# Performance work log

Hardware: AMD Instinct MI355X
Metric: run time of the kernel (lower is better)

## Reference

```python
import jax, jax.numpy as jnp
import numpy as np

D_MODEL, D_HIDDEN, N_EXPERTS = 1024, 4096, 8
CAP_FACTOR, LBL_COEF, ZLOSS_COEF = 1.25, 0.01, 0.0


def setup_inputs() -> dict:
    key = jax.random.key(0)
    ks = jax.random.split(key, 4)
    B, T = 4, 2048
    x = jax.random.normal(ks[0], (B, T, D_MODEL), dtype=jnp.float32)
    # router linear
    Wr = jax.random.normal(ks[1], (D_MODEL, N_EXPERTS), jnp.float32) / np.sqrt(D_MODEL).astype(np.float32)
    br = jnp.zeros((N_EXPERTS,), jnp.float32)
    # per-expert MLP: fc1 [D->H], gelu, fc2 [H->D]
    W1 = jax.random.normal(ks[2], (N_EXPERTS, D_MODEL, D_HIDDEN), jnp.float32) / np.sqrt(D_MODEL).astype(np.float32)
    b1 = jnp.zeros((N_EXPERTS, D_HIDDEN), jnp.float32)
    W2 = jax.random.normal(ks[3], (N_EXPERTS, D_HIDDEN, D_MODEL), jnp.float32) / np.sqrt(D_HIDDEN).astype(np.float32)
    b2 = jnp.zeros((N_EXPERTS, D_MODEL), jnp.float32)
    return {"x": x, "Wr": Wr, "br": br, "W1": W1, "b1": b1, "W2": W2, "b2": b2}


def reference(x, Wr, br, W1, b1, W2, b2):
    B, T, D = x.shape
    N = B * T
    E = Wr.shape[1]
    cap = int(CAP_FACTOR * (N / E) + 1)  # static Python int

    h = x.reshape(N, D)
    # --- Top1Router ---
    logits = h @ Wr + br                              # [N, E]
    probs = jax.nn.softmax(logits, axis=-1)
    top1 = jnp.argmax(probs, axis=-1)                 # [N]
    w = jnp.take_along_axis(probs, top1[:, None], axis=1)  # [N, 1]
    assign = jax.nn.one_hot(top1, E, dtype=jnp.float32)    # constant wrt grads
    importance = probs.mean(axis=0)
    load = jax.lax.stop_gradient(assign).mean(axis=0)
    lb_loss = E * jnp.sum(importance * load)
    z_loss = jnp.mean(jax.nn.logsumexp(logits, axis=-1) ** 2)

    # --- capacity-based dispatch (first `cap` tokens per expert, token order) ---
    pos = (jnp.cumsum(assign, axis=0) * assign).sum(axis=-1).astype(jnp.int32) - 1  # [N] slot within expert
    keep = pos < cap
    slot = jnp.where(keep, pos, cap)  # dropped tokens -> overflow slot `cap`
    xe = jnp.zeros((E, cap + 1, D), x.dtype).at[top1, slot].set(h)[:, :cap]  # [E, cap, D]

    # --- per-expert MLP as grouped GEMMs ---
    he = jax.nn.gelu(jnp.einsum('ecd,edh->ech', xe, W1) + b1[:, None, :])    # [E, cap, H]
    ye = jnp.einsum('ech,ehd->ecd', he, W2) + b2[:, None, :]                 # [E, cap, D]

    # --- combine (gather back, scale by router weight, zero dropped) ---
    out = ye[top1, jnp.minimum(pos, cap - 1)] * w   # [N, D]
    out = jnp.where(keep[:, None], out, jnp.zeros((), x.dtype))
    y = out.reshape(B, T, D)
    aux = LBL_COEF * lb_loss + ZLOSS_COEF * z_loss
    return (y, aux)
```

## Files before the change

kernel.cpp:

```cpp
#include <hip/hip_runtime.h>
#include <hip/hip_bf16.h>

#define N_TOK 8192
#define DM    1024
#define DH    4096
#define NE    8
#define CAP   1281
#define CAPR  1408

typedef unsigned short u16;
typedef __attribute__((ext_vector_type(8))) __bf16 bf16x8;
typedef __attribute__((ext_vector_type(8))) short short8;
typedef __attribute__((ext_vector_type(4))) float f4;

__device__ __forceinline__ u16 f2bf(float f){
  union { float f; unsigned u; } v; v.f = f;
  unsigned r = v.u + 0x7fffu + ((v.u >> 16) & 1u);
  return (u16)(r >> 16);
}

__device__ __forceinline__ float gelu_t(float v){
  return 0.5f * v * (1.f + tanhf(0.7978845608028654f * (v + 0.044715f * v * v * v)));
}

__device__ __forceinline__ void gl2lds16(const void* g, void* l){
  __builtin_amdgcn_global_load_lds((const __attribute__((address_space(1))) void*)g,
                                   (__attribute__((address_space(3))) void*)l, 16, 0, 0);
}

__global__ __launch_bounds__(256) void cvt_x_k(const float* __restrict__ in, u16* __restrict__ out){
  int i = blockIdx.x * 256 + threadIdx.x;
  const f4* p = (const f4*)in + (size_t)i * 2;
  f4 a = p[0], b = p[1];
  short8 o;
  o[0]=(short)f2bf(a[0]); o[1]=(short)f2bf(a[1]); o[2]=(short)f2bf(a[2]); o[3]=(short)f2bf(a[3]);
  o[4]=(short)f2bf(b[0]); o[5]=(short)f2bf(b[1]); o[6]=(short)f2bf(b[2]); o[7]=(short)f2bf(b[3]);
  *(short8*)(out + (size_t)i*8) = o;
}

__global__ __launch_bounds__(256) void tcvt_k(const float* __restrict__ in, u16* __restrict__ out,
                                              int K, int Nn){
  __shared__ float tile[64][65];
  size_t mb = (size_t)blockIdx.z * (size_t)K * (size_t)Nn;
  const float* ip = in + mb;
  u16* op = out + mb;
  int n0 = blockIdx.x*64, k0 = blockIdx.y*64;
  int tx = threadIdx.x & 63, ty = threadIdx.x >> 6;
  #pragma unroll
  for (int i=0;i<16;i++){
    int r = ty*16 + i;
    tile[r][tx] = ip[(size_t)(k0+r)*Nn + n0 + tx];
  }
  __syncthreads();
  #pragma unroll
  for (int i=0;i<16;i++){
    int r = ty*16 + i;
    op[(size_t)(n0+r)*K + k0 + tx] = f2bf(tile[tx][r]);
  }
}

__global__ __launch_bounds__(256) void router_k(const float* __restrict__ x, const float* __restrict__ Wr,
    const float* __restrict__ br, int* __restrict__ top1, float* __restrict__ wgt,
    float* __restrict__ impSum){
  __shared__ float pSh[4][8];
  int wid = threadIdx.x >> 6, lane = threadIdx.x & 63;
  int n = blockIdx.x * 4 + wid;
  const float* xr = x + (size_t)n * DM;
  float acc[8];
  #pragma unroll
  for (int e=0;e<8;e++) acc[e]=0.f;
  #pragma unroll
  for (int c=0;c<4;c++){
    int d0 = c*256 + lane*4;
    f4 xv = *(const f4*)(xr + d0);
    #pragma unroll
    for (int j=0;j<4;j++){
      const float* wrow = Wr + (size_t)(d0+j)*NE;
      float xs = xv[j];
      #pragma unroll
      for (int e=0;e<8;e++) acc[e] = fmaf(xs, wrow[e], acc[e]);
    }
  }
  #pragma unroll
  for (int off=32; off>0; off>>=1){
    #pragma unroll
    for (int e=0;e<8;e++) acc[e] += __shfl_down(acc[e], off, 64);
  }
  if (lane==0){
    float lg[8]; float mx = -1e30f;
    #pragma unroll
    for (int e=0;e<8;e++){ lg[e] = acc[e] + br[e]; mx = fmaxf(mx, lg[e]); }
    float p[8], s=0.f;
    #pragma unroll
    for (int e=0;e<8;e++){ p[e] = expf(lg[e]-mx); s += p[e]; }
    int bt=0; float bv=lg[0];
    #pragma unroll
    for (int e=1;e<8;e++){ if (lg[e]>bv){ bv=lg[e]; bt=e; } }
    float inv = 1.f/s;
    top1[n] = bt; wgt[n] = p[bt]*inv;
    #pragma unroll
    for (int e=0;e<8;e++) pSh[wid][e] = p[e]*inv;
  }
  __syncthreads();
  if (threadIdx.x < 8){
    int e = threadIdx.x;
    atomicAdd(&impSum[e], pSh[0][e]+pSh[1][e]+pSh[2][e]+pSh[3][e]);
  }
}

__global__ __launch_bounds__(1024) void scan_k(const int* __restrict__ top1, int* __restrict__ idx,
    int* __restrict__ cnt, int* __restrict__ rawcnt, int* __restrict__ dropList,
    int* __restrict__ nDrop, const float* __restrict__ impSum, float* __restrict__ auxOut){
  __shared__ int waveCnt[16][8];
  __shared__ int wavePre[16][8];
  __shared__ int chunkTot[8];
  __shared__ int base_s[8];
  int tid = threadIdx.x, wid = tid>>6, lane = tid&63;
  if (tid < 8) base_s[tid] = 0;
  __syncthreads();
  for (int c=0;c<8;c++){
    int t = c*1024 + tid;
    int e = top1[t];
    int myPre = 0;
    #pragma unroll
    for (int ex=0; ex<8; ex++){
      unsigned long long mk = __ballot(e == ex);
      if (lane == 0) waveCnt[wid][ex] = __popcll(mk);
      if (ex == e) myPre = __popcll(mk & ((1ull<<lane)-1ull));
    }
    __syncthreads();
    if (tid < 8){
      int run = 0;
      for (int wv=0; wv<16; wv++){ wavePre[wv][tid] = run; run += waveCnt[wv][tid]; }
      chunkTot[tid] = run;
    }
    __syncthreads();
    int pos = base_s[e] + wavePre[wid][e] + myPre;
    if (pos < CAP) idx[e*CAPR + pos] = t;
    else { int d = atomicAdd(nDrop, 1); dropList[d] = t; }
    __syncthreads();
    if (tid < 8) base_s[tid] += chunkTot[tid];
    __syncthreads();
  }
  if (tid < 8){
    rawcnt[tid] = base_s[tid];
    cnt[tid] = base_s[tid] < CAP ? base_s[tid] : CAP;
  }
  if (tid == 0){
    float s = 0.f;
    for (int e=0;e<8;e++) s += (impSum[e]*(1.f/N_TOK)) * ((float)base_s[e]*(1.f/N_TOK));
    *auxOut = 0.01f * 8.f * s;
  }
}

__global__ __launch_bounds__(256) void zdrop_k(const int* __restrict__ dropList,
    const int* __restrict__ nDrop, float* __restrict__ y){
  int nd = *nDrop;
  for (int i = blockIdx.x; i < nd; i += gridDim.x){
    int t = dropList[i];
    f4* row = (f4*)(y + (size_t)t * DM);
    f4 z; z[0]=0.f; z[1]=0.f; z[2]=0.f; z[3]=0.f;
    row[threadIdx.x] = z;
  }
}

__global__ __launch_bounds__(256) void gemm1_k(
    const u16* __restrict__ Xb, const u16* __restrict__ W1T,
    const float* __restrict__ b1, const int* __restrict__ idx,
    const int* __restrict__ cnt, u16* __restrict__ He)
{
  int e = blockIdx.z, mt = blockIdx.y, nt = blockIdx.x;
  int cn = cnt[e];
  if (mt*128 >= cn) return;
  __shared__ __align__(16) u16 As[128*64];
  __shared__ __align__(16) u16 Bs[128*64];
  int tid = threadIdx.x, lane = tid&63, wid = tid>>6;
  int arow = tid>>3, acb = tid&7;

  const u16* aS[4]; const u16* bS[4];
  #pragma unroll
  for (int c=0;c<4;c++){
    int row = c*32 + arow;
    int gcb = acb ^ (row&7);
    int slot = mt*128 + row;
    int token = (slot < cn) ? idx[e*CAPR + slot] : idx[e*CAPR];
    aS[c] = Xb + (size_t)token*DM + gcb*8;
    bS[c] = W1T + ((size_t)e*DH + nt*128 + row)*DM + gcb*8;
  }
  f4 acc[4][4];
  #pragma unroll
  for (int m=0;m<4;m++)
    #pragma unroll
    for (int n=0;n<4;n++)
      #pragma unroll
      for (int j=0;j<4;j++) acc[m][n][j]=0.f;

  int waveM = wid>>1, waveN = wid&1;
  int rA = lane&15, kb = lane>>4;

  for (int kt=0; kt<DM/64; kt++){
    #pragma unroll
    for (int c=0;c<4;c++){
      gl2lds16(aS[c] + kt*64, &As[c*2048 + tid*8]);
      gl2lds16(bS[c] + kt*64, &Bs[c*2048 + tid*8]);
    }
    __syncthreads();
    #pragma unroll
    for (int kk=0;kk<2;kk++){
      bf16x8 af[4], bf_[4];
      #pragma unroll
      for (int m=0;m<4;m++){
        int row = waveM*64 + m*16 + rA;
        int ch = (kk*4+kb) ^ (row&7);
        af[m] = *(const bf16x8*)&As[row*64 + ch*8];
      }
      #pragma unroll
      for (int n=0;n<4;n++){
        int col = waveN*64 + n*16 + rA;
        int ch = (kk*4+kb) ^ (col&7);
        bf_[n] = *(const bf16x8*)&Bs[col*64 + ch*8];
      }
      #pragma unroll
      for (int m=0;m<4;m++)
        #pragma unroll
        for (int n=0;n<4;n++)
          acc[m][n] = __builtin_amdgcn_mfma_f32_16x16x32_bf16(af[m], bf_[n], acc[m][n], 0,0,0);
    }
    __syncthreads();
  }
  int rG = lane>>4;
  #pragma unroll
  for (int n=0;n<4;n++){
    int col = nt*128 + waveN*64 + n*16 + rA;
    float bias = b1[e*DH + col];
    #pragma unroll
    for (int m=0;m<4;m++){
      int slot = mt*128 + waveM*64 + m*16 + rG*4;
      u16* dst = He + ((size_t)e*CAPR + slot)*DH + col;
      #pragma unroll
      for (int j=0;j<4;j++){
        float v = acc[m][n][j] + bias;
        dst[(size_t)j*DH] = f2bf(gelu_t(v));
      }
    }
  }
}

__global__ __launch_bounds__(256) void gemm2_k(
    const u16* __restrict__ He, const u16* __restrict__ W2T,
    const float* __restrict__ b2, const int* __restrict__ idx,
    const int* __restrict__ cnt, const float* __restrict__ wgt,
    float* __restrict__ y)
{
  int e = blockIdx.z, mt = blockIdx.y, nt = blockIdx.x;
  int cn = cnt[e];
  if (mt*128 >= cn) return;
  __shared__ __align__(16) u16 As[128*64];
  __shared__ __align__(16) u16 Bs[128*64];
  int tid = threadIdx.x, lane = tid&63, wid = tid>>6;
  int arow = tid>>3, acb = tid&7;

  const u16* aS[4]; const u16* bS[4];
  #pragma unroll
  for (int c=0;c<4;c++){
    int row = c*32 + arow;
    int gcb = acb ^ (row&7);
    aS[c] = He  + ((size_t)e*CAPR + mt*128 + row)*DH + gcb*8;
    bS[c] = W2T + ((size_t)e*DM   + nt*128 + row)*DH + gcb*8;
  }
  f4 acc[4][4];
  #pragma unroll
  for (int m=0;m<4;m++)
    #pragma unroll
    for (int n=0;n<4;n++)
      #pragma unroll
      for (int j=0;j<4;j++) acc[m][n][j]=0.f;

  int waveM = wid>>1, waveN = wid&1;
  int rA = lane&15, kb = lane>>4;

  for (int kt=0; kt<DH/64; kt++){
    #pragma unroll
    for (int c=0;c<4;c++){
      gl2lds16(aS[c] + kt*64, &As[c*2048 + tid*8]);
      gl2lds16(bS[c] + kt*64, &Bs[c*2048 + tid*8]);
    }
    __syncthreads();
    #pragma unroll
    for (int kk=0;kk<2;kk++){
      bf16x8 af[4], bf_[4];
      #pragma unroll
      for (int m=0;m<4;m++){
        int row = waveM*64 + m*16 + rA;
        int ch = (kk*4+kb) ^ (row&7);
        af[m] = *(const bf16x8*)&As[row*64 + ch*8];
      }
      #pragma unroll
      for (int n=0;n<4;n++){
        int col = waveN*64 + n*16 + rA;
        int ch = (kk*4+kb) ^ (col&7);
        bf_[n] = *(const bf16x8*)&Bs[col*64 + ch*8];
      }
      #pragma unroll
      for (int m=0;m<4;m++)
        #pragma unroll
        for (int n=0;n<4;n++)
          acc[m][n] = __builtin_amdgcn_mfma_f32_16x16x32_bf16(af[m], bf_[n], acc[m][n], 0,0,0);
    }
    __syncthreads();
  }
  int rG = lane>>4;
  #pragma unroll
  for (int m=0;m<4;m++){
    int slot0 = mt*128 + waveM*64 + m*16 + rG*4;
    #pragma unroll
    for (int j=0;j<4;j++){
      int slot = slot0 + j;
      bool valid = slot < cn;
      int tk = valid ? idx[e*CAPR + slot] : 0;
      float wv = valid ? wgt[tk] : 0.f;
      #pragma unroll
      for (int n=0;n<4;n++){
        int col = nt*128 + waveN*64 + n*16 + rA;
        if (valid) y[(size_t)tk*DM + col] = (acc[m][n][j] + b2[e*DM + col]) * wv;
      }
    }
  }
}

extern "C" void kernel_launch(void* const* d_in, const int* in_sizes, int n_in,
                              void* d_out, int out_size, void* d_ws, size_t ws_size,
                              hipStream_t stream){
  const float* x  = (const float*)d_in[0];
  const float* Wr = (const float*)d_in[1];
  const float* br = (const float*)d_in[2];
  const float* W1 = (const float*)d_in[3];
  const float* b1 = (const float*)d_in[4];
  const float* W2 = (const float*)d_in[5];
  const float* b2 = (const float*)d_in[6];
  float* y = (float*)d_out;

  char* ws = (char*)d_ws;
  u16* Xb  = (u16*)(ws);
  u16* W1T = (u16*)(ws + 16777216ull);
  u16* W2T = (u16*)(ws + 16777216ull + 67108864ull);
  u16* He  = (u16*)(ws + 16777216ull + 2ull*67108864ull);
  char* tail = ws + 16777216ull + 2ull*67108864ull + (size_t)NE*CAPR*DH*2ull;
  int*   top1 = (int*)(tail);
  float* wgt  = (float*)(tail + 32768);
  int*   idx  = (int*)(tail + 65536);
  int*   drop = (int*)(tail + 65536 + 45056);
  float* impSum = (float*)(tail + 65536 + 45056 + 32768);
  int*   nDrop  = (int*)((char*)impSum + 32);
  int*   cnt    = nDrop + 1;
  int*   rawcnt = cnt + 8;

  hipMemsetAsync(impSum, 0, 64, stream);

  cvt_x_k<<<4096, 256, 0, stream>>>(x, Xb);
  tcvt_k<<<dim3(64,16,8), 256, 0, stream>>>(W1, W1T, DM, DH);
  tcvt_k<<<dim3(16,64,8), 256, 0, stream>>>(W2, W2T, DH, DM);
  router_k<<<2048, 256, 0, stream>>>(x, Wr, br, top1, wgt, impSum);
  scan_k<<<1, 1024, 0, stream>>>(top1, idx, cnt, rawcnt, drop, nDrop, impSum,
                                 y + (size_t)N_TOK*DM);
  zdrop_k<<<64, 256, 0, stream>>>(drop, nDrop, y);
  gemm1_k<<<dim3(DH/128, CAPR/128, NE), 256, 0, stream>>>(Xb, W1T, b1, idx, cnt, He);
  gemm2_k<<<dim3(DM/128, CAPR/128, NE), 256, 0, stream>>>(He, W2T, b2, idx, cnt, wgt, y);

  (void)in_sizes; (void)n_in; (void)out_size; (void)ws_size;
}
```

Baseline: 378.1 us.

## Double-buffer 256x256 grouped GEMMs with phased MFMA/load overlap and faster GELU

Both expert GEMMs move from 128x128 tiles with a single LDS buffer to 256x256 tiles on 512 threads. They double-buffer LDS and interleave global-to-LDS loads with MFMA phases, using explicit barriers, waitcnt and priority hints, so load latency hides behind compute. GELU's tanh is rewritten through exp and a hardware reciprocal, and the weight-transpose kernel now does vectorized loads and stores. The index array stride is padded to 1536 so the 6 larger M tiles can read past CAPR safely. The cost is higher register and LDS pressure, plus a slightly different GELU approximation.

```diff
diff --git a/kernel.cpp b/kernel.cpp
--- a/kernel.cpp
+++ b/kernel.cpp
@@ -7,6 +7,7 @@
 #define NE    8
 #define CAP   1281
 #define CAPR  1408
+#define ISTR  1536
 
 typedef unsigned short u16;
 typedef __attribute__((ext_vector_type(8))) __bf16 bf16x8;
@@ -19,8 +20,9 @@
   return (u16)(r >> 16);
 }
 
-__device__ __forceinline__ float gelu_t(float v){
-  return 0.5f * v * (1.f + tanhf(0.7978845608028654f * (v + 0.044715f * v * v * v)));
+__device__ __forceinline__ float gelu_fast(float v){
+  float u = 0.7978845608028654f * (v + 0.044715f * v * v * v);
+  return v * __builtin_amdgcn_rcpf(1.0f + __expf(-2.0f * u));
 }
 
 __device__ __forceinline__ void gl2lds16(const void* g, void* l){
@@ -40,23 +42,29 @@
 
 __global__ __launch_bounds__(256) void tcvt_k(const float* __restrict__ in, u16* __restrict__ out,
                                               int K, int Nn){
-  __shared__ float tile[64][65];
+  __shared__ float tile[64][68];
   size_t mb = (size_t)blockIdx.z * (size_t)K * (size_t)Nn;
   const float* ip = in + mb;
   u16* op = out + mb;
   int n0 = blockIdx.x*64, k0 = blockIdx.y*64;
-  int tx = threadIdx.x & 63, ty = threadIdx.x >> 6;
-  #pragma unroll
-  for (int i=0;i<16;i++){
-    int r = ty*16 + i;
-    tile[r][tx] = ip[(size_t)(k0+r)*Nn + n0 + tx];
+  int t = threadIdx.x;
+  int kr = t>>4, nc = (t&15)*4;
+  #pragma unroll
+  for (int ii=0;ii<4;ii++){
+    f4 v = *(const f4*)&ip[(size_t)(k0+kr+16*ii)*Nn + n0 + nc];
+    tile[kr+16*ii][nc+0] = v[0]; tile[kr+16*ii][nc+1] = v[1];
+    tile[kr+16*ii][nc+2] = v[2]; tile[kr+16*ii][nc+3] = v[3];
   }
   __syncthreads();
-  #pragma unroll
-  for (int i=0;i<16;i++){
-    int r = ty*16 + i;
-    op[(size_t)(n0+r)*K + k0 + tx] = f2bf(tile[tx][r]);
-  }
+  int nr = t>>2, kc = (t&3)*16;
+  short8 o0, o1;
+  #pragma unroll
+  for (int c=0;c<8;c++){
+    o0[c] = (short)f2bf(tile[kc+c][nr]);
+    o1[c] = (short)f2bf(tile[kc+8+c][nr]);
+  }
+  *(short8*)&op[(size_t)(n0+nr)*K + k0 + kc] = o0;
+  *(short8*)&op[(size_t)(n0+nr)*K + k0 + kc + 8] = o1;
 }
 
 __global__ __launch_bounds__(256) void router_k(const float* __restrict__ x, const float* __restrict__ Wr,
@@ -136,7 +144,7 @@
     }
     __syncthreads();
     int pos = base_s[e] + wavePre[wid][e] + myPre;
-    if (pos < CAP) idx[e*CAPR + pos] = t;
+    if (pos < CAP) idx[e*ISTR + pos] = t;
     else { int d = atomicAdd(nDrop, 1); dropList[d] = t; }
     __syncthreads();
     if (tid < 8) base_s[tid] += chunkTot[tid];
@@ -164,89 +172,119 @@
   }
 }
 
-__global__ __launch_bounds__(256) void gemm1_k(
+#define SA(buf, h, kt) do{ \
+  gl2lds16(aS[(h)*2+0] + (size_t)(kt)*64, &lds[(buf)*16384 + ((h)*2+0)*4096 + t*8]); \
+  gl2lds16(aS[(h)*2+1] + (size_t)(kt)*64, &lds[(buf)*16384 + ((h)*2+1)*4096 + t*8]); }while(0)
+#define SBg(buf, h, kt) do{ \
+  gl2lds16(bS[(h)*2+0] + (size_t)(kt)*64, &lds[32768 + (buf)*16384 + ((h)*2+0)*4096 + t*8]); \
+  gl2lds16(bS[(h)*2+1] + (size_t)(kt)*64, &lds[32768 + (buf)*16384 + ((h)*2+1)*4096 + t*8]); }while(0)
+
+#define LDA(buf, m, kk) (*(const bf16x8*)&lds[(buf)*16384 + (aBase ^ ((kk)*32)) + (m)*1024])
+#define LDB(buf, n, kk) (*(const bf16x8*)&lds[32768 + (buf)*16384 + (bBase ^ ((kk)*32)) + (n)*1024])
+
+#define PHASE(buf, q, STAGES, PREBAR) do{ \
+  bf16x8 a_[2][2]; \
+  if ((q)==0){ \
+    _Pragma("unroll") for (int n_=0;n_<4;n_++) \
+      _Pragma("unroll") for (int kk_=0;kk_<2;kk_++) Bf[n_][kk_] = LDB(buf, n_, kk_); \
+  } \
+  _Pragma("unroll") for (int j_=0;j_<2;j_++) \
+    _Pragma("unroll") for (int kk_=0;kk_<2;kk_++) a_[j_][kk_] = LDA(buf, 2*(q)+j_, kk_); \
+  STAGES; \
+  __builtin_amdgcn_s_barrier(); \
+  asm volatile("s_waitcnt lgkmcnt(0)" ::: "memory"); \
+  __builtin_amdgcn_sched_barrier(0); \
+  __builtin_amdgcn_s_setprio(1); \
+  _Pragma("unroll") for (int j_=0;j_<2;j_++) \
+    _Pragma("unroll") for (int n_=0;n_<4;n_++) \
+      _Pragma("unroll") for (int kk_=0;kk_<2;kk_++) \
+        acc[2*(q)+j_][n_] = __builtin_amdgcn_mfma_f32_16x16x32_bf16(a_[j_][kk_], Bf[n_][kk_], acc[2*(q)+j_][n_], 0,0,0); \
+  __builtin_amdgcn_s_setprio(0); \
+  PREBAR; \
+  __builtin_amdgcn_s_barrier(); \
+}while(0)
+
+#define VMC4 asm volatile("s_waitcnt vmcnt(4)" ::: "memory")
+#define NOP2 (void)0
+
+__global__ __launch_bounds__(512, 2) void gemm1_k(
     const u16* __restrict__ Xb, const u16* __restrict__ W1T,
     const float* __restrict__ b1, const int* __restrict__ idx,
     const int* __restrict__ cnt, u16* __restrict__ He)
 {
   int e = blockIdx.z, mt = blockIdx.y, nt = blockIdx.x;
   int cn = cnt[e];
-  if (mt*128 >= cn) return;
-  __shared__ __align__(16) u16 As[128*64];
-  __shared__ __align__(16) u16 Bs[128*64];
-  int tid = threadIdx.x, lane = tid&63, wid = tid>>6;
-  int arow = tid>>3, acb = tid&7;
+  if (mt*256 >= cn) return;
+  __shared__ __align__(16) u16 lds[65536];
+  int t = threadIdx.x, lane = t&63, wid = t>>6;
+  int waveM = wid>>2, waveN = wid&3;
+  int rA = lane&15, kb = lane>>4, s = rA&7;
 
   const u16* aS[4]; const u16* bS[4];
   #pragma unroll
-  for (int c=0;c<4;c++){
-    int row = c*32 + arow;
-    int gcb = acb ^ (row&7);
-    int slot = mt*128 + row;
-    int token = (slot < cn) ? idx[e*CAPR + slot] : idx[e*CAPR];
-    aS[c] = Xb + (size_t)token*DM + gcb*8;
-    bS[c] = W1T + ((size_t)e*DH + nt*128 + row)*DM + gcb*8;
-  }
-  f4 acc[4][4];
-  #pragma unroll
-  for (int m=0;m<4;m++)
+  for (int j=0;j<4;j++){
+    int pos = j*512 + t;
+    int row = pos>>3, ch = pos&7;
+    int gcb = ch ^ (row&7);
+    int slotrow = mt*256 + row;
+    int token = (slotrow < cn) ? idx[e*ISTR + slotrow] : 0;
+    aS[j] = Xb + (size_t)token*DM + gcb*8;
+    bS[j] = W1T + ((size_t)e*DH + nt*256 + row)*DM + gcb*8;
+  }
+  f4 acc[8][4];
+  #pragma unroll
+  for (int m=0;m<8;m++)
     #pragma unroll
     for (int n=0;n<4;n++)
       #pragma unroll
       for (int j=0;j<4;j++) acc[m][n][j]=0.f;
 
-  int waveM = wid>>1, waveN = wid&1;
-  int rA = lane&15, kb = lane>>4;
-
-  for (int kt=0; kt<DM/64; kt++){
-    #pragma unroll
-    for (int c=0;c<4;c++){
-      gl2lds16(aS[c] + kt*64, &As[c*2048 + tid*8]);
-      gl2lds16(bS[c] + kt*64, &Bs[c*2048 + tid*8]);
-    }
-    __syncthreads();
-    #pragma unroll
-    for (int kk=0;kk<2;kk++){
-      bf16x8 af[4], bf_[4];
-      #pragma unroll
-      for (int m=0;m<4;m++){
-        int row = waveM*64 + m*16 + rA;
-        int ch = (kk*4+kb) ^ (row&7);
-        af[m] = *(const bf16x8*)&As[row*64 + ch*8];
-      }
-      #pragma unroll
-      for (int n=0;n<4;n++){
-        int col = waveN*64 + n*16 + rA;
-        int ch = (kk*4+kb) ^ (col&7);
-        bf_[n] = *(const bf16x8*)&Bs[col*64 + ch*8];
-      }
-      #pragma unroll
-      for (int m=0;m<4;m++)
+  int aBase = (waveM*128 + rA)*64 + (kb ^ s)*8;
+  int bBase = (waveN*64  + rA)*64 + (kb ^ s)*8;
+  bf16x8 Bf[4][2];
+
+  SBg(0,0,0); SBg(0,1,0); SA(0,0,0); SA(0,1,0); SBg(1,0,1); SBg(1,1,1);
+  VMC4;
+  __builtin_amdgcn_s_barrier();
+
+  const int NT = DM/64;
+  #pragma unroll 1
+  for (int i=0;i<NT/2;i++){
+    int kt1 = 2*i+1;
+    int kt2 = (2*i+2 < NT) ? 2*i+2 : NT-1;
+    int kt3 = (2*i+3 < NT) ? 2*i+3 : NT-1;
+    PHASE(0,0, SA(1,0,kt1), NOP2);
+    PHASE(0,1, { SA(1,1,kt1); SBg(0,0,kt2); }, NOP2);
+    PHASE(0,2, SBg(0,1,kt2), NOP2);
+    PHASE(0,3, NOP2, VMC4);
+    PHASE(1,0, SA(0,0,kt2), NOP2);
+    PHASE(1,1, { SA(0,1,kt2); SBg(1,0,kt3); }, NOP2);
+    PHASE(1,2, SBg(1,1,kt3), NOP2);
+    PHASE(1,3, NOP2, VMC4);
+  }
+  asm volatile("s_waitcnt vmcnt(0)" ::: "memory");
+
+  int rG = lane>>4;
+  #pragma unroll
+  for (int n=0;n<4;n++){
+    int col = nt*256 + waveN*64 + n*16 + rA;
+    float bias = b1[e*DH + col];
+    #pragma unroll
+    for (int m=0;m<8;m++){
+      int slot = mt*256 + waveM*128 + m*16 + rG*4;
+      if (slot < CAPR){
+        u16* dst = He + ((size_t)e*CAPR + slot)*DH + col;
         #pragma unroll
-        for (int n=0;n<4;n++)
-          acc[m][n] = __builtin_amdgcn_mfma_f32_16x16x32_bf16(af[m], bf_[n], acc[m][n], 0,0,0);
-    }
-    __syncthreads();
-  }
-  int rG = lane>>4;
-  #pragma unroll
-  for (int n=0;n<4;n++){
-    int col = nt*128 + waveN*64 + n*16 + rA;
-    float bias = b1[e*DH + col];
-    #pragma unroll
-    for (int m=0;m<4;m++){
-      int slot = mt*128 + waveM*64 + m*16 + rG*4;
-      u16* dst = He + ((size_t)e*CAPR + slot)*DH + col;
-      #pragma unroll
-      for (int j=0;j<4;j++){
-        float v = acc[m][n][j] + bias;
-        dst[(size_t)j*DH] = f2bf(gelu_t(v));
+        for (int j=0;j<4;j++){
+          float v = acc[m][n][j] + bias;
+          dst[(size_t)j*DH] = f2bf(gelu_fast(v));
+        }
       }
     }
   }
 }
 
-__global__ __launch_bounds__(256) void gemm2_k(
+__global__ __launch_bounds__(512, 2) void gemm2_k(
     const u16* __restrict__ He, const u16* __restrict__ W2T,
     const float* __restrict__ b2, const int* __restrict__ idx,
     const int* __restrict__ cnt, const float* __restrict__ wgt,
@@ -254,75 +292,73 @@
 {
   int e = blockIdx.z, mt = blockIdx.y, nt = blockIdx.x;
   int cn = cnt[e];
-  if (mt*128 >= cn) return;
-  __shared__ __align__(16) u16 As[128*64];
-  __shared__ __align__(16) u16 Bs[128*64];
-  int tid = threadIdx.x, lane = tid&63, wid = tid>>6;
-  int arow = tid>>3, acb = tid&7;
+  if (mt*256 >= cn) return;
+  __shared__ __align__(16) u16 lds[65536];
+  int t = threadIdx.x, lane = t&63, wid = t>>6;
+  int waveM = wid>>2, waveN = wid&3;
+  int rA = lane&15, kb = lane>>4, s = rA&7;
 
   const u16* aS[4]; const u16* bS[4];
   #pragma unroll
-  for (int c=0;c<4;c++){
-    int row = c*32 + arow;
-    int gcb = acb ^ (row&7);
-    aS[c] = He  + ((size_t)e*CAPR + mt*128 + row)*DH + gcb*8;
-    bS[c] = W2T + ((size_t)e*DM   + nt*128 + row)*DH + gcb*8;
-  }
-  f4 acc[4][4];
-  #pragma unroll
-  for (int m=0;m<4;m++)
+  for (int j=0;j<4;j++){
+    int pos = j*512 + t;
+    int row = pos>>3, ch = pos&7;
+    int gcb = ch ^ (row&7);
+    int srow = mt*256 + row; if (srow >= cn) srow = cn-1;
+    aS[j] = He  + ((size_t)e*CAPR + srow)*DH + gcb*8;
+    bS[j] = W2T + ((size_t)e*DM + nt*256 + row)*DH + gcb*8;
+  }
+  f4 acc[8][4];
+  #pragma unroll
+  for (int m=0;m<8;m++)
     #pragma unroll
     for (int n=0;n<4;n++)
       #pragma unroll
       for (int j=0;j<4;j++) acc[m][n][j]=0.f;
 
-  int waveM = wid>>1, waveN = wid&1;
-  int rA = lane&15, kb = lane>>4;
-
-  for (int kt=0; kt<DH/64; kt++){
-    #pragma unroll
-    for (int c=0;c<4;c++){
-      gl2lds16(aS[c] + kt*64, &As[c*2048 + tid*8]);
-      gl2lds16(bS[c] + kt*64, &Bs[c*2048 + tid*8]);
-    }
-    __syncthreads();
-    #pragma unroll
-    for (int kk=0;kk<2;kk++){
-      bf16x8 af[4], bf_[4];
-      #pragma unroll
-      for (int m=0;m<4;m++){
-        int row = waveM*64 + m*16 + rA;
-        int ch = (kk*4+kb) ^ (row&7);
-        af[m] = *(const bf16x8*)&As[row*64 + ch*8];
-      }
-      #pragma unroll
-      for (int n=0;n<4;n++){
-        int col = waveN*64 + n*16 + rA;
-        int ch = (kk*4+kb) ^ (col&7);
-        bf_[n] = *(const bf16x8*)&Bs[col*64 + ch*8];
-      }
-      #pragma unroll
-      for (int m=0;m<4;m++)
-        #pragma unroll
-        for (int n=0;n<4;n++)
-          acc[m][n] = __builtin_amdgcn_mfma_f32_16x16x32_bf16(af[m], bf_[n], acc[m][n], 0,0,0);
-    }
-    __syncthreads();
-  }
+  int aBase = (waveM*128 + rA)*64 + (kb ^ s)*8;
+  int bBase = (waveN*64  + rA)*64 + (kb ^ s)*8;
+  bf16x8 Bf[4][2];
+
+  SBg(0,0,0); SBg(0,1,0); SA(0,0,0); SA(0,1,0); SBg(1,0,1); SBg(1,1,1);
+  VMC4;
+  __builtin_amdgcn_s_barrier();
+
+  const int NT = DH/64;
+  #pragma unroll 1
+  for (int i=0;i<NT/2;i++){
+    int kt1 = 2*i+1;
+    int kt2 = (2*i+2 < NT) ? 2*i+2 : NT-1;
+    int kt3 = (2*i+3 < NT) ? 2*i+3 : NT-1;
+    PHASE(0,0, SA(1,0,kt1), NOP2);
+    PHASE(0,1, { SA(1,1,kt1); SBg(0,0,kt2); }, NOP2);
+    PHASE(0,2, SBg(0,1,kt2), NOP2);
+    PHASE(0,3, NOP2, VMC4);
+    PHASE(1,0, SA(0,0,kt2), NOP2);
+    PHASE(1,1, { SA(0,1,kt2); SBg(1,0,kt3); }, NOP2);
+    PHASE(1,2, SBg(1,1,kt3), NOP2);
+    PHASE(1,3, NOP2, VMC4);
+  }
+  asm volatile("s_waitcnt vmcnt(0)" ::: "memory");
+
   int rG = lane>>4;
-  #pragma unroll
-  for (int m=0;m<4;m++){
-    int slot0 = mt*128 + waveM*64 + m*16 + rG*4;
+  float bias_[4];
+  #pragma unroll
+  for (int n=0;n<4;n++) bias_[n] = b2[e*DM + nt*256 + waveN*64 + n*16 + rA];
+  #pragma unroll
+  for (int m=0;m<8;m++){
+    int slot0 = mt*256 + waveM*128 + m*16 + rG*4;
     #pragma unroll
     for (int j=0;j<4;j++){
       int slot = slot0 + j;
       bool valid = slot < cn;
-      int tk = valid ? idx[e*CAPR + slot] : 0;
+      int tk = valid ? idx[e*ISTR + slot] : 0;
       float wv = valid ? wgt[tk] : 0.f;
+      float* yr = y + (size_t)tk*DM;
       #pragma unroll
       for (int n=0;n<4;n++){
-        int col = nt*128 + waveN*64 + n*16 + rA;
-        if (valid) y[(size_t)tk*DM + col] = (acc[m][n][j] + b2[e*DM + col]) * wv;
+        int col = nt*256 + waveN*64 + n*16 + rA;
+        if (valid) yr[col] = (acc[m][n][j] + bias_[n]) * wv;
       }
     }
   }
@@ -349,8 +385,8 @@
   int*   top1 = (int*)(tail);
   float* wgt  = (float*)(tail + 32768);
   int*   idx  = (int*)(tail + 65536);
-  int*   drop = (int*)(tail + 65536 + 45056);
-  float* impSum = (float*)(tail + 65536 + 45056 + 32768);
+  int*   drop = (int*)(tail + 65536 + 49152);
+  float* impSum = (float*)(tail + 65536 + 49152 + 32768);
   int*   nDrop  = (int*)((char*)impSum + 32);
   int*   cnt    = nDrop + 1;
   int*   rawcnt = cnt + 8;
@@ -364,8 +400,8 @@
   scan_k<<<1, 1024, 0, stream>>>(top1, idx, cnt, rawcnt, drop, nDrop, impSum,
                                  y + (size_t)N_TOK*DM);
   zdrop_k<<<64, 256, 0, stream>>>(drop, nDrop, y);
-  gemm1_k<<<dim3(DH/128, CAPR/128, NE), 256, 0, stream>>>(Xb, W1T, b1, idx, cnt, He);
-  gemm2_k<<<dim3(DM/128, CAPR/128, NE), 256, 0, stream>>>(He, W2T, b2, idx, cnt, wgt, y);
+  gemm1_k<<<dim3(DH/256, 6, NE), 512, 0, stream>>>(Xb, W1T, b1, idx, cnt, He);
+  gemm2_k<<<dim3(DM/256, 6, NE), 512, 0, stream>>>(He, W2T, b2, idx, cnt, wgt, y);
 
   (void)in_sizes; (void)n_in; (void)out_size; (void)ws_size;
 }
```

After: 376.1 us. Within noise of the previous version (-0.5%).
